# Optimization experiments

Measured on AMD Instinct MI355X. Metric: run time of the kernel, lower is better.

Reference implementation:

```python
import jax, jax.numpy as jnp
import numpy as np

T = 2048            # context_length
C = 1024            # embedding size
HEAD_QK = 256       # config.head_qk_size
VOCAB = 50257       # config.vocab_size


def setup_inputs() -> dict:
    key = jax.random.key(0)
    k1, k2, k3, k4 = jax.random.split(key, 4)
    x = jax.random.normal(k1, (T, C), dtype=jnp.float32)
    idx = jax.random.randint(k2, (T,), 0, VOCAB, dtype=jnp.int32)
    # Dense kernels (flax Dense stores kernel as [in, out], no bias)
    Wq = jax.random.normal(k3, (C, HEAD_QK), dtype=jnp.float32) / np.sqrt(C)
    Wk = jax.random.normal(k4, (C, HEAD_QK), dtype=jnp.float32) / np.sqrt(C)
    return {"x": x, "idx": idx, "Wq": Wq, "Wk": Wk}


def reference(x, idx, Wq, Wk):
    # q, k: [T, HEAD_QK]
    q = x @ Wq
    k = x @ Wk
    # causal-masked, softmax-free scores: [T, T]
    c = (q @ k.T) * (1.0 / HEAD_QK)
    causal = jnp.tril(jnp.ones((T, T), dtype=bool))
    c = jnp.where(causal, c, 0.0)
    # c @ one_hot(idx, VOCAB) == segment-sum of c's columns by token id
    # out[t, v] = sum_{s : idx[s] == v} c[t, s]   -> [T, VOCAB]
    out = jax.ops.segment_sum(c.T, idx, num_segments=VOCAB).T
    return out
```

## Files before the change

kernel.cpp:

```cpp
#include <hip/hip_runtime.h>

#define T_CTX 2048
#define C_DIM 1024
#define HQK   256
#define NVOC  50257
#define NBMW  394

typedef float nfloat4 __attribute__((ext_vector_type(4)));
typedef _Float16 h2 __attribute__((ext_vector_type(2)));
typedef _Float16 h4 __attribute__((ext_vector_type(4)));
typedef _Float16 h8 __attribute__((ext_vector_type(8)));
typedef float f32x4 __attribute__((ext_vector_type(4)));

#if defined(__has_builtin)
#if __has_builtin(__builtin_amdgcn_fdot2)
#define HAVE_FDOT2 1
#endif
#endif
__device__ __forceinline__ float fdot2acc(h2 a, h2 b, float c) {
#ifdef HAVE_FDOT2
    return __builtin_amdgcn_fdot2(a, b, c, false);
#else
    return c + (float)a.x * (float)b.x + (float)a.y * (float)b.y;
#endif
}

__global__ __launch_bounds__(1024) void k_build_first(const int* __restrict__ idx,
                                                      int* __restrict__ first,
                                                      int* __restrict__ vocab_map,
                                                      unsigned* __restrict__ bm) {
    __shared__ int sidx[T_CTX];
    __shared__ int skey[4096];
    __shared__ int sval[4096];
    __shared__ unsigned sbm[NBMW];
    const int tid = threadIdx.x;
    for (int i = tid; i < T_CTX; i += 1024) sidx[i] = idx[i];
    for (int i = tid; i < 4096; i += 1024) { skey[i] = -1; sval[i] = 0x7fffffff; }
    for (int i = tid; i < NBMW; i += 1024) sbm[i] = 0u;
    int4* vm4 = reinterpret_cast<int4*>(vocab_map);
    const int4 neg1 = make_int4(-1, -1, -1, -1);
    for (int i = tid; i < 12564; i += 1024) vm4[i] = neg1;
    if (tid == 0) vocab_map[NVOC - 1] = -1;
    __syncthreads();
#pragma unroll
    for (int rep = 0; rep < 2; ++rep) {
        const int s = tid + rep * 1024;
        const int my = sidx[s];
        int h = (int)(((unsigned)my * 2654435761u) >> 16) & 4095;
        while (true) {
            int k = skey[h];
            if (k == my) break;
            if (k == -1) {
                int old = atomicCAS(&skey[h], -1, my);
                if (old == -1 || old == my) break;
            }
            h = (h + 1) & 4095;
        }
        atomicMin(&sval[h], s);
    }
    __syncthreads();
#pragma unroll
    for (int rep = 0; rep < 2; ++rep) {
        const int s = tid + rep * 1024;
        const int my = sidx[s];
        int h = (int)(((unsigned)my * 2654435761u) >> 16) & 4095;
        while (skey[h] != my) h = (h + 1) & 4095;
        const int mp = sval[h];
        first[s] = mp;
        if (mp == s) {
            vocab_map[my] = s;
            const int qd = my >> 2;
            atomicOr(&sbm[qd >> 5], 1u << (qd & 31));
        }
    }
    __syncthreads();
    for (int i = tid; i < NBMW; i += 1024) bm[i] = sbm[i];
}

__global__ __launch_bounds__(512) void k_gemm_qk(const float* __restrict__ x,
                                                 const float* __restrict__ Wq,
                                                 const float* __restrict__ Wk,
                                                 _Float16* __restrict__ qbuf_h,
                                                 _Float16* __restrict__ kbuf_h) {
    __shared__ h2 As2[16 * 68];
    __shared__ _Float16 BsH[16 * 136];
    const int row0 = blockIdx.x * 64;
    const int col0 = blockIdx.y * 64;
    const bool is_q = (col0 < HQK);
    const float* __restrict__ W = is_q ? Wq : Wk;
    _Float16* __restrict__ obuf = is_q ? qbuf_h : kbuf_h;
    const int wc0 = is_q ? col0 : (col0 - HQK);
    const int tid = threadIdx.x;
    const int tr = (tid >> 4) << 1;
    const int tc = (tid & 15) << 2;
    const int ar = tid >> 3, ak = (tid & 7) << 2;
    const int bk = tid >> 4, bc = (tid & 15) << 2;
    float acc[2][4] = {};
    for (int k0 = 0; k0 < C_DIM; k0 += 32) {
        float4 a4 = *reinterpret_cast<const float4*>(&x[(size_t)(row0 + ar) * C_DIM + k0 + ak]);
        float4 b4 = *reinterpret_cast<const float4*>(&W[(size_t)(k0 + bk) * HQK + wc0 + bc]);
        As2[(ak >> 1) * 68 + ar]       = h2{(_Float16)a4.x, (_Float16)a4.y};
        As2[((ak >> 1) + 1) * 68 + ar] = h2{(_Float16)a4.z, (_Float16)a4.w};
        {
            const int r = (bk >> 1) * 136, p = bk & 1;
            BsH[r + ((bc + 0) << 1) + p] = (_Float16)b4.x;
            BsH[r + ((bc + 1) << 1) + p] = (_Float16)b4.y;
            BsH[r + ((bc + 2) << 1) + p] = (_Float16)b4.z;
            BsH[r + ((bc + 3) << 1) + p] = (_Float16)b4.w;
        }
        __syncthreads();
#pragma unroll
        for (int kk2 = 0; kk2 < 16; ++kk2) {
            h2 a0 = As2[kk2 * 68 + tr];
            h2 a1 = As2[kk2 * 68 + tr + 1];
            const h2* bp = reinterpret_cast<const h2*>(&BsH[kk2 * 136 + (tc << 1)]);
            h2 b0 = bp[0], b1 = bp[1], b2 = bp[2], b3 = bp[3];
            acc[0][0] = fdot2acc(a0, b0, acc[0][0]); acc[0][1] = fdot2acc(a0, b1, acc[0][1]);
            acc[0][2] = fdot2acc(a0, b2, acc[0][2]); acc[0][3] = fdot2acc(a0, b3, acc[0][3]);
            acc[1][0] = fdot2acc(a1, b0, acc[1][0]); acc[1][1] = fdot2acc(a1, b1, acc[1][1]);
            acc[1][2] = fdot2acc(a1, b2, acc[1][2]); acc[1][3] = fdot2acc(a1, b3, acc[1][3]);
        }
        __syncthreads();
    }
#pragma unroll
    for (int i = 0; i < 2; ++i) {
        h4 o = {(_Float16)acc[i][0], (_Float16)acc[i][1], (_Float16)acc[i][2], (_Float16)acc[i][3]};
        *reinterpret_cast<h4*>(&obuf[(size_t)(row0 + tr + i) * HQK + wc0 + tc]) = o;
    }
}

__global__ __launch_bounds__(256) void k_scores_mfma(const _Float16* __restrict__ q,
                                                     const _Float16* __restrict__ kb,
                                                     float* __restrict__ c) {
    const int bt = blockIdx.x, bs = blockIdx.y;
    if (bs > bt) return;
    const int row0 = bt * 64, col0 = bs * 64;
    const int w = threadIdx.x >> 6;
    const int lane = threadIdx.x & 63;
    const int arow = row0 + 16 * w + (lane & 15);
    const int kgrp = (lane >> 4) << 3;
    f32x4 acc[4] = {};
#pragma unroll
    for (int k0 = 0; k0 < HQK; k0 += 32) {
        h8 a = *reinterpret_cast<const h8*>(&q[(size_t)arow * HQK + k0 + kgrp]);
#pragma unroll
        for (int ct = 0; ct < 4; ++ct) {
            h8 b = *reinterpret_cast<const h8*>(&kb[(size_t)(col0 + 16 * ct + (lane & 15)) * HQK + k0 + kgrp]);
            acc[ct] = __builtin_amdgcn_mfma_f32_16x16x32_f16(a, b, acc[ct], 0, 0, 0);
        }
    }
    const float scale = 1.0f / 256.0f;
    const int orow = row0 + 16 * w + ((lane >> 4) << 2);
    const int ocol = col0 + (lane & 15);
#pragma unroll
    for (int ct = 0; ct < 4; ++ct)
#pragma unroll
        for (int r = 0; r < 4; ++r)
            c[(size_t)(orow + r) * T_CTX + ocol + 16 * ct] = acc[ct][r] * scale;
}

__global__ __launch_bounds__(256) void k_fold_expand(const float* __restrict__ c,
                                                     const int* __restrict__ first,
                                                     const int* __restrict__ vocab_map,
                                                     const unsigned* __restrict__ bm,
                                                     float* __restrict__ out) {
    __shared__ float rowc[T_CTX];
    __shared__ unsigned sbm[NBMW];
    const int t = blockIdx.x;
    for (int i = threadIdx.x; i < T_CTX; i += 256) rowc[i] = 0.0f;
    for (int i = threadIdx.x; i < NBMW; i += 256) sbm[i] = bm[i];
    __syncthreads();
    const int nq = (t >> 2) + 1;
    for (int qd = threadIdx.x; qd < nq; qd += 256) {
        const int s0 = qd << 2;
        float4 v = *reinterpret_cast<const float4*>(&c[(size_t)t * T_CTX + s0]);
        int4 f4 = *reinterpret_cast<const int4*>(&first[s0]);
        if (s0 + 3 <= t) {
            atomicAdd(&rowc[f4.x], v.x); atomicAdd(&rowc[f4.y], v.y);
            atomicAdd(&rowc[f4.z], v.z); atomicAdd(&rowc[f4.w], v.w);
        } else {
            atomicAdd(&rowc[f4.x], v.x);
            if (s0 + 1 <= t) atomicAdd(&rowc[f4.y], v.y);
            if (s0 + 2 <= t) atomicAdd(&rowc[f4.z], v.z);
            if (s0 + 3 <= t) atomicAdd(&rowc[f4.w], v.w);
        }
    }
    __syncthreads();
    float* __restrict__ orow = out + (size_t)t * NVOC;
    const int lead = (4 - (t & 3)) & 3;
    if ((int)threadIdx.x < lead) {
        int m = vocab_map[threadIdx.x];
        orow[threadIdx.x] = (m >= 0) ? rowc[m] : 0.0f;
    }
    const int nvec = (NVOC - lead) >> 2;
    const nfloat4 z4 = {0.0f, 0.0f, 0.0f, 0.0f};
    for (int i = threadIdx.x; i < nvec; i += 256) {
        const int v = lead + (i << 2);
        const int q0 = v >> 2, q1 = (v + 3) >> 2;
        const unsigned hit = ((sbm[q0 >> 5] >> (q0 & 31)) | (sbm[q1 >> 5] >> (q1 & 31))) & 1u;
        if (hit) {
            int m0 = vocab_map[v + 0], m1 = vocab_map[v + 1];
            int m2 = vocab_map[v + 2], m3 = vocab_map[v + 3];
            nfloat4 o;
            o.x = (m0 >= 0) ? rowc[m0] : 0.0f;
            o.y = (m1 >= 0) ? rowc[m1] : 0.0f;
            o.z = (m2 >= 0) ? rowc[m2] : 0.0f;
            o.w = (m3 >= 0) ? rowc[m3] : 0.0f;
            __builtin_nontemporal_store(o, reinterpret_cast<nfloat4*>(&orow[v]));
        } else {
            __builtin_nontemporal_store(z4, reinterpret_cast<nfloat4*>(&orow[v]));
        }
    }
    for (int v = lead + (nvec << 2) + threadIdx.x; v < NVOC; v += 256) {
        int m = vocab_map[v];
        orow[v] = (m >= 0) ? rowc[m] : 0.0f;
    }
}

extern "C" void kernel_launch(void* const* d_in, const int* in_sizes, int n_in,
                              void* d_out, int out_size, void* d_ws, size_t ws_size,
                              hipStream_t stream) {
    const float* x   = (const float*)d_in[0];
    const int*   idx = (const int*)d_in[1];
    const float* Wq  = (const float*)d_in[2];
    const float* Wk  = (const float*)d_in[3];
    float* out = (float*)d_out;

    char* ws = (char*)d_ws;
    _Float16* qbuf_h   = (_Float16*)(ws);
    _Float16* kbuf_h   = (_Float16*)(ws + (1u << 20));
    float*    c        = (float*)(ws + (2u << 20));
    int*      first    = (int*)(ws + (18u << 20));
    int*      vocab_map = (int*)(ws + (18u << 20) + (16u << 10));
    unsigned* bm       = (unsigned*)(ws + (19u << 20));

    k_build_first<<<1, 1024, 0, stream>>>(idx, first, vocab_map, bm);
    dim3 gg(32, 8);
    k_gemm_qk<<<gg, 512, 0, stream>>>(x, Wq, Wk, qbuf_h, kbuf_h);
    dim3 gs(32, 32);
    k_scores_mfma<<<gs, 256, 0, stream>>>(qbuf_h, kbuf_h, c);
    k_fold_expand<<<T_CTX, 256, 0, stream>>>(c, first, vocab_map, bm, out);
}
```

Measured before the change: 536.6 us.

## Merge token-map build into projection kernel and store scores in fp16

The single-block token-dedup/hash kernel becomes an extra block (index 256) of the Q/K projection kernel, so both run in one launch and the hash build overlaps the GEMM instead of running serially. The intermediate score matrix c is written and read as fp16 instead of fp32, halving its traffic between the scores and fold kernels. The cost is lower precision in the scores before the fp32 accumulation. Shared memory is now a single union buffer sized for the larger of the two roles.

```diff
diff --git a/kernel.cpp b/kernel.cpp
--- a/kernel.cpp
+++ b/kernel.cpp
@@ -25,72 +25,71 @@
 #endif
 }
 
-__global__ __launch_bounds__(1024) void k_build_first(const int* __restrict__ idx,
-                                                      int* __restrict__ first,
-                                                      int* __restrict__ vocab_map,
-                                                      unsigned* __restrict__ bm) {
-    __shared__ int sidx[T_CTX];
-    __shared__ int skey[4096];
-    __shared__ int sval[4096];
-    __shared__ unsigned sbm[NBMW];
+__global__ __launch_bounds__(512) void k_proj_build(const float* __restrict__ x,
+                                                    const float* __restrict__ Wq,
+                                                    const float* __restrict__ Wk,
+                                                    const int* __restrict__ idx,
+                                                    _Float16* __restrict__ qbuf_h,
+                                                    _Float16* __restrict__ kbuf_h,
+                                                    int* __restrict__ first,
+                                                    int* __restrict__ vocab_map,
+                                                    unsigned* __restrict__ bm) {
+    __shared__ __align__(16) int smem_i[10640];
     const int tid = threadIdx.x;
-    for (int i = tid; i < T_CTX; i += 1024) sidx[i] = idx[i];
-    for (int i = tid; i < 4096; i += 1024) { skey[i] = -1; sval[i] = 0x7fffffff; }
-    for (int i = tid; i < NBMW; i += 1024) sbm[i] = 0u;
-    int4* vm4 = reinterpret_cast<int4*>(vocab_map);
-    const int4 neg1 = make_int4(-1, -1, -1, -1);
-    for (int i = tid; i < 12564; i += 1024) vm4[i] = neg1;
-    if (tid == 0) vocab_map[NVOC - 1] = -1;
-    __syncthreads();
-#pragma unroll
-    for (int rep = 0; rep < 2; ++rep) {
-        const int s = tid + rep * 1024;
-        const int my = sidx[s];
-        int h = (int)(((unsigned)my * 2654435761u) >> 16) & 4095;
-        while (true) {
-            int k = skey[h];
-            if (k == my) break;
-            if (k == -1) {
-                int old = atomicCAS(&skey[h], -1, my);
-                if (old == -1 || old == my) break;
+
+    if (blockIdx.x == 256) {
+        int* sidx = smem_i;
+        int* skey = smem_i + 2048;
+        int* sval = smem_i + 6144;
+        unsigned* sbm = (unsigned*)(smem_i + 10240);
+        for (int i = tid; i < T_CTX; i += 512) sidx[i] = idx[i];
+        for (int i = tid; i < 4096; i += 512) { skey[i] = -1; sval[i] = 0x7fffffff; }
+        for (int i = tid; i < NBMW; i += 512) sbm[i] = 0u;
+        int4* vm4 = reinterpret_cast<int4*>(vocab_map);
+        const int4 neg1 = make_int4(-1, -1, -1, -1);
+        for (int i = tid; i < 12564; i += 512) vm4[i] = neg1;
+        if (tid == 0) vocab_map[NVOC - 1] = -1;
+        __syncthreads();
+        for (int s = tid; s < T_CTX; s += 512) {
+            const int my = sidx[s];
+            int h = (int)(((unsigned)my * 2654435761u) >> 16) & 4095;
+            while (true) {
+                int k = skey[h];
+                if (k == my) break;
+                if (k == -1) {
+                    int old = atomicCAS(&skey[h], -1, my);
+                    if (old == -1 || old == my) break;
+                }
+                h = (h + 1) & 4095;
             }
-            h = (h + 1) & 4095;
-        }
-        atomicMin(&sval[h], s);
-    }
-    __syncthreads();
-#pragma unroll
-    for (int rep = 0; rep < 2; ++rep) {
-        const int s = tid + rep * 1024;
-        const int my = sidx[s];
-        int h = (int)(((unsigned)my * 2654435761u) >> 16) & 4095;
-        while (skey[h] != my) h = (h + 1) & 4095;
-        const int mp = sval[h];
-        first[s] = mp;
-        if (mp == s) {
-            vocab_map[my] = s;
-            const int qd = my >> 2;
-            atomicOr(&sbm[qd >> 5], 1u << (qd & 31));
-        }
-    }
-    __syncthreads();
-    for (int i = tid; i < NBMW; i += 1024) bm[i] = sbm[i];
-}
-
-__global__ __launch_bounds__(512) void k_gemm_qk(const float* __restrict__ x,
-                                                 const float* __restrict__ Wq,
-                                                 const float* __restrict__ Wk,
-                                                 _Float16* __restrict__ qbuf_h,
-                                                 _Float16* __restrict__ kbuf_h) {
-    __shared__ h2 As2[16 * 68];
-    __shared__ _Float16 BsH[16 * 136];
-    const int row0 = blockIdx.x * 64;
-    const int col0 = blockIdx.y * 64;
+            atomicMin(&sval[h], s);
+        }
+        __syncthreads();
+        for (int s = tid; s < T_CTX; s += 512) {
+            const int my = sidx[s];
+            int h = (int)(((unsigned)my * 2654435761u) >> 16) & 4095;
+            while (skey[h] != my) h = (h + 1) & 4095;
+            const int mp = sval[h];
+            first[s] = mp;
+            if (mp == s) {
+                vocab_map[my] = s;
+                const int qd = my >> 2;
+                atomicOr(&sbm[qd >> 5], 1u << (qd & 31));
+            }
+        }
+        __syncthreads();
+        for (int i = tid; i < NBMW; i += 512) bm[i] = sbm[i];
+        return;
+    }
+
+    h2* As2 = reinterpret_cast<h2*>(smem_i);
+    _Float16* BsH = reinterpret_cast<_Float16*>(smem_i + 1088);
+    const int row0 = (blockIdx.x >> 3) * 64;
+    const int col0 = (blockIdx.x & 7) * 64;
     const bool is_q = (col0 < HQK);
     const float* __restrict__ W = is_q ? Wq : Wk;
     _Float16* __restrict__ obuf = is_q ? qbuf_h : kbuf_h;
     const int wc0 = is_q ? col0 : (col0 - HQK);
-    const int tid = threadIdx.x;
     const int tr = (tid >> 4) << 1;
     const int tc = (tid & 15) << 2;
     const int ar = tid >> 3, ak = (tid & 7) << 2;
@@ -131,7 +130,7 @@
 
 __global__ __launch_bounds__(256) void k_scores_mfma(const _Float16* __restrict__ q,
                                                      const _Float16* __restrict__ kb,
-                                                     float* __restrict__ c) {
+                                                     _Float16* __restrict__ c) {
     const int bt = blockIdx.x, bs = blockIdx.y;
     if (bs > bt) return;
     const int row0 = bt * 64, col0 = bs * 64;
@@ -156,10 +155,10 @@
     for (int ct = 0; ct < 4; ++ct)
 #pragma unroll
         for (int r = 0; r < 4; ++r)
-            c[(size_t)(orow + r) * T_CTX + ocol + 16 * ct] = acc[ct][r] * scale;
-}
-
-__global__ __launch_bounds__(256) void k_fold_expand(const float* __restrict__ c,
+            c[(size_t)(orow + r) * T_CTX + ocol + 16 * ct] = (_Float16)(acc[ct][r] * scale);
+}
+
+__global__ __launch_bounds__(256) void k_fold_expand(const _Float16* __restrict__ c,
                                                      const int* __restrict__ first,
                                                      const int* __restrict__ vocab_map,
                                                      const unsigned* __restrict__ bm,
@@ -173,16 +172,16 @@
     const int nq = (t >> 2) + 1;
     for (int qd = threadIdx.x; qd < nq; qd += 256) {
         const int s0 = qd << 2;
-        float4 v = *reinterpret_cast<const float4*>(&c[(size_t)t * T_CTX + s0]);
+        h4 v = *reinterpret_cast<const h4*>(&c[(size_t)t * T_CTX + s0]);
         int4 f4 = *reinterpret_cast<const int4*>(&first[s0]);
         if (s0 + 3 <= t) {
-            atomicAdd(&rowc[f4.x], v.x); atomicAdd(&rowc[f4.y], v.y);
-            atomicAdd(&rowc[f4.z], v.z); atomicAdd(&rowc[f4.w], v.w);
+            atomicAdd(&rowc[f4.x], (float)v.x); atomicAdd(&rowc[f4.y], (float)v.y);
+            atomicAdd(&rowc[f4.z], (float)v.z); atomicAdd(&rowc[f4.w], (float)v.w);
         } else {
-            atomicAdd(&rowc[f4.x], v.x);
-            if (s0 + 1 <= t) atomicAdd(&rowc[f4.y], v.y);
-            if (s0 + 2 <= t) atomicAdd(&rowc[f4.z], v.z);
-            if (s0 + 3 <= t) atomicAdd(&rowc[f4.w], v.w);
+            atomicAdd(&rowc[f4.x], (float)v.x);
+            if (s0 + 1 <= t) atomicAdd(&rowc[f4.y], (float)v.y);
+            if (s0 + 2 <= t) atomicAdd(&rowc[f4.z], (float)v.z);
+            if (s0 + 3 <= t) atomicAdd(&rowc[f4.w], (float)v.w);
         }
     }
     __syncthreads();
@@ -229,14 +228,13 @@
     char* ws = (char*)d_ws;
     _Float16* qbuf_h   = (_Float16*)(ws);
     _Float16* kbuf_h   = (_Float16*)(ws + (1u << 20));
-    float*    c        = (float*)(ws + (2u << 20));
-    int*      first    = (int*)(ws + (18u << 20));
-    int*      vocab_map = (int*)(ws + (18u << 20) + (16u << 10));
-    unsigned* bm       = (unsigned*)(ws + (19u << 20));
-
-    k_build_first<<<1, 1024, 0, stream>>>(idx, first, vocab_map, bm);
-    dim3 gg(32, 8);
-    k_gemm_qk<<<gg, 512, 0, stream>>>(x, Wq, Wk, qbuf_h, kbuf_h);
+    _Float16* c        = (_Float16*)(ws + (2u << 20));
+    int*      first    = (int*)(ws + (10u << 20));
+    int*      vocab_map = (int*)(ws + (10u << 20) + (16u << 10));
+    unsigned* bm       = (unsigned*)(ws + (11u << 20));
+
+    k_proj_build<<<257, 512, 0, stream>>>(x, Wq, Wk, idx, qbuf_h, kbuf_h,
+                                          first, vocab_map, bm);
     dim3 gs(32, 32);
     k_scores_mfma<<<gs, 256, 0, stream>>>(qbuf_h, kbuf_h, c);
     k_fold_expand<<<T_CTX, 256, 0, stream>>>(c, first, vocab_map, bm, out);
```

Measured after the change: 525.9 us. 1.02x faster.
